# Kernel optimization log

Measured on AMD Instinct MI355X. Metric: run time of the kernel, lower is better.

Reference implementation:

```python
import jax, jax.numpy as jnp
import numpy as np

E = 8        # num_experts
TOPK = 2     # k
D = 1024     # input/output size
H = 4096     # expert hidden size


def setup_inputs() -> dict:
    key = jax.random.key(0)
    ks = jax.random.split(key, 8)
    s = 0.02
    return {
        "hidden_states": jax.random.normal(ks[0], (2, 2048, D), dtype=jnp.float32),
        "Wr": jax.random.normal(ks[1], (D, E), dtype=jnp.float32) * s,
        "br": jnp.zeros((E,), dtype=jnp.float32),
        "gate_bias": jnp.zeros((E,), dtype=jnp.float32),
        "W1": jax.random.normal(ks[2], (E, D, H), dtype=jnp.float32) * s,
        "b1": jnp.zeros((E, H), dtype=jnp.float32),
        "W2": jax.random.normal(ks[3], (E, H, D), dtype=jnp.float32) * s,
        "b2": jnp.zeros((E, D), dtype=jnp.float32),
    }


def reference(hidden_states, Wr, br, gate_bias, W1, b1, W2, b2):
    B, S, Din = hidden_states.shape
    x = hidden_states.reshape(B * S, Din)              # [T, D]
    # Router: logits + gate bias, top-k, softmax over the k selected logits
    logits = x @ Wr + br + gate_bias                   # [T, E]
    top_v, top_i = jax.lax.top_k(logits, TOPK)         # [T, k]
    probs = jax.nn.softmax(top_v, axis=-1)             # [T, k]
    # Scatter top-k probs into dense per-expert gate weights [T, E]
    gate = jnp.einsum("tk,tke->te", probs,
                      jax.nn.one_hot(top_i, E, dtype=probs.dtype))
    # Per-expert MLP (exact gelu, eval mode -> no dropout/noise),
    # weighted-combine; zero gate weight == token not routed to expert.
    out = jnp.zeros((B * S, W2.shape[-1]), dtype=x.dtype)
    for e in range(E):
        h = jax.nn.gelu(x @ W1[e] + b1[e], approximate=False)  # [T, H]
        y = h @ W2[e] + b2[e]                                  # [T, D]
        out = out + gate[:, e:e + 1] * y
    return out.reshape(B, S, -1)
```

## Files before the change

kernel.cpp:

```cpp
#include <hip/hip_runtime.h>
#include <hip/hip_bf16.h>
#include <stdint.h>
#include <stddef.h>


#define T_TOK 4096
#define DIM   1024
#define HID   4096
#define NE    8
#define MT_MAX 40

typedef unsigned short u16;
typedef __bf16 bf16x8 __attribute__((ext_vector_type(8)));
typedef float  f32x4  __attribute__((ext_vector_type(4)));
typedef u16    u16x8  __attribute__((ext_vector_type(8)));

__device__ __forceinline__ u16 f2bf(float f) {
  union { float f; uint32_t u; } v; v.f = f;
  uint32_t u = v.u;
  return (u16)((u + 0x7fffu + ((u >> 16) & 1u)) >> 16);
}

__global__ void router_kernel(const float* __restrict__ x, const float* __restrict__ Wr,
                              const float* __restrict__ br, const float* __restrict__ gb,
                              int* __restrict__ counts, int* __restrict__ lists,
                              float* __restrict__ gate_p) {
  const int t = blockIdx.x * 4 + (threadIdx.x >> 6);
  const int lane = threadIdx.x & 63;
  const float* xr = x + (size_t)t * DIM;
  float acc[NE];
#pragma unroll
  for (int e = 0; e < NE; ++e) acc[e] = 0.f;
#pragma unroll
  for (int i = 0; i < DIM / 64; ++i) {
    const int k = i * 64 + lane;
    const float xv = xr[k];
    const float4 w0 = *reinterpret_cast<const float4*>(Wr + (size_t)k * NE);
    const float4 w1 = *reinterpret_cast<const float4*>(Wr + (size_t)k * NE + 4);
    acc[0] += xv * w0.x; acc[1] += xv * w0.y; acc[2] += xv * w0.z; acc[3] += xv * w0.w;
    acc[4] += xv * w1.x; acc[5] += xv * w1.y; acc[6] += xv * w1.z; acc[7] += xv * w1.w;
  }
#pragma unroll
  for (int off = 32; off >= 1; off >>= 1) {
#pragma unroll
    for (int e = 0; e < NE; ++e) acc[e] += __shfl_xor(acc[e], off);
  }
  if (lane == 0) {
    float lg[NE];
#pragma unroll
    for (int e = 0; e < NE; ++e) lg[e] = acc[e] + br[e] + gb[e];
    int i0 = 0;
#pragma unroll
    for (int e = 1; e < NE; ++e) if (lg[e] > lg[i0]) i0 = e;
    int i1 = (i0 == 0) ? 1 : 0;
#pragma unroll
    for (int e = 0; e < NE; ++e) if (e != i0 && lg[e] > lg[i1]) i1 = e;
    const float ev = expf(lg[i1] - lg[i0]);
    const float p0 = 1.f / (1.f + ev);
    const float p1 = ev / (1.f + ev);
    const int pos0 = atomicAdd(&counts[i0], 1);
    lists[i0 * T_TOK + pos0] = t * 2 + 0;
    const int pos1 = atomicAdd(&counts[i1], 1);
    lists[i1 * T_TOK + pos1] = t * 2 + 1;
    gate_p[t * 2 + 0] = p0;
    gate_p[t * 2 + 1] = p1;
  }
}

__global__ void tile_table_kernel(const int* __restrict__ counts, int* __restrict__ tab) {
  if (threadIdx.x == 0) {
    int tot = 0;
    for (int e = 0; e < NE; ++e) {
      const int c = counts[e];
      const int nt = (c + 255) >> 8;
      for (int i = 0; i < nt && tot < MT_MAX; ++i) {
        tab[tot * 2] = e; tab[tot * 2 + 1] = i * 256; ++tot;
      }
    }
    for (; tot < MT_MAX; ++tot) tab[tot * 2] = -1;
  }
}

__global__ void cvt_x_kernel(const float* __restrict__ in, u16* __restrict__ out, int n8) {
  const int i = blockIdx.x * blockDim.x + threadIdx.x;
  if (i >= n8) return;
  const float4 a = reinterpret_cast<const float4*>(in)[2 * i];
  const float4 b = reinterpret_cast<const float4*>(in)[2 * i + 1];
  u16x8 r;
  r[0] = f2bf(a.x); r[1] = f2bf(a.y); r[2] = f2bf(a.z); r[3] = f2bf(a.w);
  r[4] = f2bf(b.x); r[5] = f2bf(b.y); r[6] = f2bf(b.z); r[7] = f2bf(b.w);
  *reinterpret_cast<u16x8*>(out + (size_t)i * 8) = r;
}

__global__ void cvt_w_kernel(const float* __restrict__ in, u16* __restrict__ out,
                             int K, int N) {
  __shared__ float tile[64][65];
  const int e = blockIdx.z;
  const int n0 = blockIdx.x * 64, k0 = blockIdx.y * 64;
  const int tid = threadIdx.x;
  const float* src = in + (size_t)e * K * N;
#pragma unroll
  for (int r = 0; r < 16; ++r) {
    const int kr = r * 4 + (tid >> 6);
    tile[kr][tid & 63] = src[(size_t)(k0 + kr) * N + n0 + (tid & 63)];
  }
  __syncthreads();
  u16* dst = out + (size_t)e * N * K;
#pragma unroll
  for (int r = 0; r < 8; ++r) {
    const int nr = r * 8 + (tid >> 5);
    const int kc = (tid & 31) * 2;
    ushort2 v;
    v.x = f2bf(tile[kc][nr]);
    v.y = f2bf(tile[kc + 1][nr]);
    *reinterpret_cast<ushort2*>(&dst[(size_t)(n0 + nr) * K + k0 + kc]) = v;
  }
}

__device__ __forceinline__ void ld_afrags(const u16* sm, int cA, int fmh, int wm,
                                          int l15, int swz0, int swz1, bf16x8 af[4][2]) {
#pragma unroll
  for (int f = 0; f < 4; ++f) {
    const int r = fmh * 128 + wm * 64 + f * 16 + l15;
    af[f][0] = *reinterpret_cast<const bf16x8*>(&sm[cA + r * 64 + swz0 * 8]);
    af[f][1] = *reinterpret_cast<const bf16x8*>(&sm[cA + r * 64 + swz1 * 8]);
  }
}
__device__ __forceinline__ void ld_bfrags(const u16* sm, int cA, int nfh, int wn,
                                          int l15, int swz0, int swz1, bf16x8 bfr[2][2]) {
#pragma unroll
  for (int g = 0; g < 2; ++g) {
    const int r = nfh * 128 + wn * 32 + g * 16 + l15;
    bfr[g][0] = *reinterpret_cast<const bf16x8*>(&sm[32768 + cA + r * 64 + swz0 * 8]);
    bfr[g][1] = *reinterpret_cast<const bf16x8*>(&sm[32768 + cA + r * 64 + swz1 * 8]);
  }
}
__device__ __forceinline__ void wr_half(u16* sm, int baseoff, int h, int trow, int wslot,
                                        const bf16x8 v[2]) {
#pragma unroll
  for (int j = 0; j < 2; ++j) {
    const int r = h * 128 + j * 64 + trow;
    *reinterpret_cast<bf16x8*>(&sm[baseoff + r * 64 + wslot * 8]) = v[j];
  }
}

#define PH_SYNC()                                           \
  asm volatile("s_waitcnt lgkmcnt(0)" ::: "memory");        \
  __builtin_amdgcn_s_barrier();                             \
  __builtin_amdgcn_sched_barrier(0);

#define MMQ(FMH, NFH, AF, BF)                                                   \
  __builtin_amdgcn_s_setprio(1);                                                \
  _Pragma("unroll") for (int f_ = 0; f_ < 4; ++f_)                              \
  _Pragma("unroll") for (int g_ = 0; g_ < 2; ++g_)                              \
  _Pragma("unroll") for (int ks_ = 0; ks_ < 2; ++ks_)                           \
    acc[(FMH) * 4 + f_][(NFH) * 2 + g_] =                                       \
        __builtin_amdgcn_mfma_f32_16x16x32_bf16(                                \
            AF[f_][ks_], BF[g_][ks_], acc[(FMH) * 4 + f_][(NFH) * 2 + g_],      \
            0, 0, 0);                                                           \
  __builtin_amdgcn_s_setprio(0);

template <int KT, int NT, int NSPLIT, int PHASE>
__global__ __launch_bounds__(512, 2)
void gemm_kernel(const u16* __restrict__ Abase, const u16* __restrict__ Bt,
                 const float* __restrict__ bias, const int* __restrict__ counts,
                 const int* __restrict__ lists, const float* __restrict__ gate_p,
                 const int* __restrict__ tab,
                 u16* __restrict__ hout, float* __restrict__ yout) {
  const int e = tab[blockIdx.x * 2];
  if (e < 0) return;
  const int m0 = tab[blockIdx.x * 2 + 1];
  const int cnt = counts[e];
  const int n0 = blockIdx.y * 256;
  const int z = blockIdx.z;
  const int kbase = z * (KT / NSPLIT);
  constexpr int nkt = (KT / NSPLIT) / 64;

  const int tid = threadIdx.x;
  const int lane = tid & 63, w = tid >> 6;
  const int wm = w >> 2, wn = w & 3;
  const int l15 = lane & 15, lks = lane >> 4;
  const int rb = l15 & 7;
  const int swz0 = lks ^ rb, swz1 = (4 + lks) ^ rb;

  __shared__ alignas(16) u16 lds[65536];
  __shared__ int rowp[256];

  if (tid < 256) {
    const int idx = m0 + tid;
    rowp[tid] = lists[e * T_TOK + (idx < cnt ? idx : cnt - 1)];
  }
  __syncthreads();

  const int trow = tid >> 3;
  const int tslot = tid & 7;
  const int wslot = tslot ^ (trow & 7);
  const u16* aP[2][2];
  const u16* bP[2][2];
#pragma unroll
  for (int h = 0; h < 2; ++h)
#pragma unroll
    for (int j = 0; j < 2; ++j) {
      const int r = h * 128 + j * 64 + trow;
      const int p = rowp[r];
      const int arow = (PHASE == 1) ? (p >> 1) : p;
      aP[h][j] = Abase + (size_t)arow * KT + kbase + tslot * 8;
      bP[h][j] = Bt + ((size_t)e * NT + n0 + r) * KT + kbase + tslot * 8;
    }

  f32x4 acc[8][4];
#pragma unroll
  for (int a = 0; a < 8; ++a)
#pragma unroll
    for (int b = 0; b < 4; ++b) acc[a][b] = f32x4{0.f, 0.f, 0.f, 0.f};

  bf16x8 aL0[2], aL1[2], bL0[2], bL1[2], af[4][2], bfr[2][2];

  {
    bf16x8 w0[2], w1[2];
#pragma unroll
    for (int j = 0; j < 2; ++j) {
      w0[j]  = *reinterpret_cast<const bf16x8*>(aP[0][j]);
      w1[j]  = *reinterpret_cast<const bf16x8*>(bP[0][j]);
      aL1[j] = *reinterpret_cast<const bf16x8*>(aP[1][j]);
      bL1[j] = *reinterpret_cast<const bf16x8*>(bP[1][j]);
    }
    wr_half(lds, 0, 0, trow, wslot, w0);
    wr_half(lds, 32768, 0, trow, wslot, w1);
  }

#define TILE(C, T)                                                                   \
  {                                                                                  \
    constexpr int cA = (C) * 16384;                                                  \
    constexpr int nA = ((C) ^ 1) * 16384;                                            \
    const int tn = (T) + 1;                                                          \
                                       \
    PH_SYNC();                                                                       \
    ld_afrags(lds, cA, 0, wm, l15, swz0, swz1, af);                                  \
    ld_bfrags(lds, cA, 0, wn, l15, swz0, swz1, bfr);                                 \
    if (tn < nkt) {                                                                  \
      aL0[0] = *reinterpret_cast<const bf16x8*>(aP[0][0] + tn * 64);                 \
      aL0[1] = *reinterpret_cast<const bf16x8*>(aP[0][1] + tn * 64);                 \
    }                                                                                \
    wr_half(lds, 32768 + cA, 1, trow, wslot, bL1);                                   \
    MMQ(0, 0, af, bfr);                                                              \
                                          \
    PH_SYNC();                                                                       \
    ld_bfrags(lds, cA, 1, wn, l15, swz0, swz1, bfr);                                 \
    if (tn < nkt) {                                                                  \
      bL0[0] = *reinterpret_cast<const bf16x8*>(bP[0][0] + tn * 64);                 \
      bL0[1] = *reinterpret_cast<const bf16x8*>(bP[0][1] + tn * 64);                 \
    }                                                                                \
    wr_half(lds, cA, 1, trow, wslot, aL1);                                           \
    MMQ(0, 1, af, bfr);                                                              \
                                      \
    PH_SYNC();                                                                       \
    ld_afrags(lds, cA, 1, wm, l15, swz0, swz1, af);                                  \
    ld_bfrags(lds, cA, 0, wn, l15, swz0, swz1, bfr);                                 \
    if (tn < nkt) {                                                                  \
      bL1[0] = *reinterpret_cast<const bf16x8*>(bP[1][0] + tn * 64);                 \
      bL1[1] = *reinterpret_cast<const bf16x8*>(bP[1][1] + tn * 64);                 \
    }                                                                                \
    wr_half(lds, nA, 0, trow, wslot, aL0);                                           \
    MMQ(1, 0, af, bfr);                                                              \
                            \
    ld_bfrags(lds, cA, 1, wn, l15, swz0, swz1, bfr);                                 \
    if (tn < nkt) {                                                                  \
      aL1[0] = *reinterpret_cast<const bf16x8*>(aP[1][0] + tn * 64);                 \
      aL1[1] = *reinterpret_cast<const bf16x8*>(aP[1][1] + tn * 64);                 \
    }                                                                                \
    wr_half(lds, 32768 + nA, 0, trow, wslot, bL0);                                   \
    MMQ(1, 1, af, bfr);                                                              \
  }

  for (int t = 0; t < nkt; t += 2) {
    TILE(0, t);
    TILE(1, t + 1);
  }
#undef TILE

  const float* bias_e = bias + (size_t)e * NT;
  const float bz = (z == 0) ? 1.f : 0.f;
#pragma unroll
  for (int fm = 0; fm < 8; ++fm) {
    const int rbase = (fm >> 2) * 128 + wm * 64 + (fm & 3) * 16 + (lane >> 4) * 4;
#pragma unroll
    for (int r = 0; r < 4; ++r) {
      const int row = rbase + r;
      if (m0 + row >= cnt) continue;
      const int p = rowp[row];
#pragma unroll
      for (int nf = 0; nf < 4; ++nf) {
        const int n = n0 + (nf >> 1) * 128 + wn * 32 + (nf & 1) * 16 + l15;
        const float v = acc[fm][nf][r];
        if (PHASE == 1) {
          const float vb = v + bias_e[n];
          const float g = 0.5f * vb * (1.0f + erff(vb * 0.70710678118654752f));
          hout[(size_t)p * NT + n] = f2bf(g);
        } else if (PHASE == 2) {
          yout[(size_t)z * T_TOK * 2 * NT + (size_t)p * NT + n] =
              gate_p[p] * (v + bz * bias_e[n]);
        } else {
          atomicAdd(&yout[(size_t)(p >> 1) * NT + n], gate_p[p] * (v + bz * bias_e[n]));
        }
      }
    }
  }
}

__global__ void combine4_kernel(const float* __restrict__ yp, float* __restrict__ out) {
  const int i = blockIdx.x * blockDim.x + threadIdx.x;
  const int t = i >> 8, d4 = i & 255;
  const size_t r0 = (size_t)(2 * t) * 256 + d4;
  const size_t zoff = (size_t)T_TOK * 2 * DIM / 4;
  const float4 a = reinterpret_cast<const float4*>(yp)[r0];
  const float4 b = reinterpret_cast<const float4*>(yp)[r0 + 256];
  const float4 c = reinterpret_cast<const float4*>(yp)[zoff + r0];
  const float4 d = reinterpret_cast<const float4*>(yp)[zoff + r0 + 256];
  float4 o;
  o.x = a.x + b.x + c.x + d.x; o.y = a.y + b.y + c.y + d.y;
  o.z = a.z + b.z + c.z + d.z; o.w = a.w + b.w + c.w + d.w;
  reinterpret_cast<float4*>(out)[i] = o;
}

extern "C" void kernel_launch(void* const* d_in, const int* in_sizes, int n_in,
                              void* d_out, int out_size, void* d_ws, size_t ws_size,
                              hipStream_t stream) {
  const float* x  = (const float*)d_in[0];
  const float* Wr = (const float*)d_in[1];
  const float* br = (const float*)d_in[2];
  const float* gb = (const float*)d_in[3];
  const float* W1 = (const float*)d_in[4];
  const float* b1 = (const float*)d_in[5];
  const float* W2 = (const float*)d_in[6];
  const float* b2 = (const float*)d_in[7];
  float* out = (float*)d_out;

  char* ws = (char*)d_ws;
  size_t off = 0;
  int*   counts = (int*)(ws + off);   off += 256;
  int*   ttab   = (int*)(ws + off);   off += 512;
  int*   lists  = (int*)(ws + off);   off += (size_t)NE * T_TOK * 4;
  float* gate_p = (float*)(ws + off); off += (size_t)T_TOK * 2 * 4;
  u16*   xb     = (u16*)(ws + off);   off += (size_t)T_TOK * DIM * 2;
  u16*   wbuf   = (u16*)(ws + off);   off += (size_t)NE * DIM * HID * 2;
  u16*   hbuf   = (u16*)(ws + off);   off += (size_t)T_TOK * 2 * HID * 2;
  float* ypair  = (float*)(ws + off);
  const size_t need_full = off + (size_t)2 * T_TOK * 2 * DIM * 4;
  const bool use_ypair = (ws_size >= need_full);

  hipMemsetAsync(counts, 0, 32, stream);
  router_kernel<<<T_TOK / 4, 256, 0, stream>>>(x, Wr, br, gb, counts, lists, gate_p);
  tile_table_kernel<<<1, 64, 0, stream>>>(counts, ttab);
  cvt_x_kernel<<<(T_TOK * DIM / 8 + 255) / 256, 256, 0, stream>>>(x, xb, T_TOK * DIM / 8);
  cvt_w_kernel<<<dim3(HID / 64, DIM / 64, NE), 256, 0, stream>>>(W1, wbuf, DIM, HID);
  gemm_kernel<DIM, HID, 1, 1><<<dim3(MT_MAX, HID / 256, 1), 512, 0, stream>>>(
      xb, wbuf, b1, counts, lists, gate_p, ttab, hbuf, nullptr);
  cvt_w_kernel<<<dim3(DIM / 64, HID / 64, NE), 256, 0, stream>>>(W2, wbuf, HID, DIM);
  if (use_ypair) {
    gemm_kernel<HID, DIM, 2, 2><<<dim3(MT_MAX, DIM / 256, 2), 512, 0, stream>>>(
        hbuf, wbuf, b2, counts, lists, gate_p, ttab, nullptr, ypair);
    combine4_kernel<<<T_TOK * DIM / 4 / 256, 256, 0, stream>>>(ypair, out);
  } else {
    hipMemsetAsync(out, 0, (size_t)out_size * 4, stream);
    gemm_kernel<HID, DIM, 2, 3><<<dim3(MT_MAX, DIM / 256, 2), 512, 0, stream>>>(
        hbuf, wbuf, b2, counts, lists, gate_p, ttab, nullptr, out);
  }
}
```

Baseline: 500.2 us.

## Stream GEMM tiles into LDS with direct global_load_lds and restructured warp mapping

Replaces the register-staged global->LDS copy in the expert GEMM main loop with direct global_load_lds async loads, double-buffered across K tiles with vmcnt-based waits and barriers between MFMA quarters. The warp-to-tile mapping also changes: each wave now owns a contiguous 128-row by 64-column block, with the epilogue index math updated to match. The aim is to free VGPRs, drop the LDS write instructions, and overlap memory traffic with MFMA work. The risk is that the hand-tuned vmcnt counts and barrier placement are fragile and could be wrong or stall.

```diff
diff --git a/kernel.cpp b/kernel.cpp
--- a/kernel.cpp
+++ b/kernel.cpp
@@ -19,6 +19,12 @@
   union { float f; uint32_t u; } v; v.f = f;
   uint32_t u = v.u;
   return (u16)((u + 0x7fffu + ((u >> 16) & 1u)) >> 16);
+}
+
+__device__ __forceinline__ void async_load16(const void* g, void* l) {
+  typedef __attribute__((address_space(1))) void GPtr;
+  typedef __attribute__((address_space(3))) void LPtr;
+  __builtin_amdgcn_global_load_lds((GPtr*)g, (LPtr*)l, 16, 0, 0);
 }
 
 __global__ void router_kernel(const float* __restrict__ x, const float* __restrict__ Wr,
@@ -116,49 +122,6 @@
     *reinterpret_cast<ushort2*>(&dst[(size_t)(n0 + nr) * K + k0 + kc]) = v;
   }
 }
-
-__device__ __forceinline__ void ld_afrags(const u16* sm, int cA, int fmh, int wm,
-                                          int l15, int swz0, int swz1, bf16x8 af[4][2]) {
-#pragma unroll
-  for (int f = 0; f < 4; ++f) {
-    const int r = fmh * 128 + wm * 64 + f * 16 + l15;
-    af[f][0] = *reinterpret_cast<const bf16x8*>(&sm[cA + r * 64 + swz0 * 8]);
-    af[f][1] = *reinterpret_cast<const bf16x8*>(&sm[cA + r * 64 + swz1 * 8]);
-  }
-}
-__device__ __forceinline__ void ld_bfrags(const u16* sm, int cA, int nfh, int wn,
-                                          int l15, int swz0, int swz1, bf16x8 bfr[2][2]) {
-#pragma unroll
-  for (int g = 0; g < 2; ++g) {
-    const int r = nfh * 128 + wn * 32 + g * 16 + l15;
-    bfr[g][0] = *reinterpret_cast<const bf16x8*>(&sm[32768 + cA + r * 64 + swz0 * 8]);
-    bfr[g][1] = *reinterpret_cast<const bf16x8*>(&sm[32768 + cA + r * 64 + swz1 * 8]);
-  }
-}
-__device__ __forceinline__ void wr_half(u16* sm, int baseoff, int h, int trow, int wslot,
-                                        const bf16x8 v[2]) {
-#pragma unroll
-  for (int j = 0; j < 2; ++j) {
-    const int r = h * 128 + j * 64 + trow;
-    *reinterpret_cast<bf16x8*>(&sm[baseoff + r * 64 + wslot * 8]) = v[j];
-  }
-}
-
-#define PH_SYNC()                                           \
-  asm volatile("s_waitcnt lgkmcnt(0)" ::: "memory");        \
-  __builtin_amdgcn_s_barrier();                             \
-  __builtin_amdgcn_sched_barrier(0);
-
-#define MMQ(FMH, NFH, AF, BF)                                                   \
-  __builtin_amdgcn_s_setprio(1);                                                \
-  _Pragma("unroll") for (int f_ = 0; f_ < 4; ++f_)                              \
-  _Pragma("unroll") for (int g_ = 0; g_ < 2; ++g_)                              \
-  _Pragma("unroll") for (int ks_ = 0; ks_ < 2; ++ks_)                           \
-    acc[(FMH) * 4 + f_][(NFH) * 2 + g_] =                                       \
-        __builtin_amdgcn_mfma_f32_16x16x32_bf16(                                \
-            AF[f_][ks_], BF[g_][ks_], acc[(FMH) * 4 + f_][(NFH) * 2 + g_],      \
-            0, 0, 0);                                                           \
-  __builtin_amdgcn_s_setprio(0);
 
 template <int KT, int NT, int NSPLIT, int PHASE>
 __global__ __launch_bounds__(512, 2)
@@ -175,13 +138,13 @@
   const int z = blockIdx.z;
   const int kbase = z * (KT / NSPLIT);
   constexpr int nkt = (KT / NSPLIT) / 64;
+  constexpr int niter = nkt / 2;
 
   const int tid = threadIdx.x;
   const int lane = tid & 63, w = tid >> 6;
   const int wm = w >> 2, wn = w & 3;
+  const int bh = wn >> 1, bs = wn & 1;
   const int l15 = lane & 15, lks = lane >> 4;
-  const int rb = l15 & 7;
-  const int swz0 = lks ^ rb, swz1 = (4 + lks) ^ rb;
 
   __shared__ alignas(16) u16 lds[65536];
   __shared__ int rowp[256];
@@ -192,98 +155,134 @@
   }
   __syncthreads();
 
-  const int trow = tid >> 3;
-  const int tslot = tid & 7;
-  const int wslot = tslot ^ (trow & 7);
-  const u16* aP[2][2];
-  const u16* bP[2][2];
+  const int sslot = (tid & 7) ^ ((tid >> 3) & 7);
+  const u16* aPtr[2][2];
+  const u16* bPtr[2][2];
 #pragma unroll
   for (int h = 0; h < 2; ++h)
 #pragma unroll
-    for (int j = 0; j < 2; ++j) {
-      const int r = h * 128 + j * 64 + trow;
+    for (int s = 0; s < 2; ++s) {
+      const int r = h * 128 + s * 64 + (tid >> 3);
       const int p = rowp[r];
       const int arow = (PHASE == 1) ? (p >> 1) : p;
-      aP[h][j] = Abase + (size_t)arow * KT + kbase + tslot * 8;
-      bP[h][j] = Bt + ((size_t)e * NT + n0 + r) * KT + kbase + tslot * 8;
+      aPtr[h][s] = Abase + (size_t)arow * KT + kbase + sslot * 8;
+      bPtr[h][s] = Bt + ((size_t)e * NT + n0 + r) * KT + kbase + sslot * 8;
     }
 
+  int aoff[2];
+#pragma unroll
+  for (int k = 0; k < 2; ++k)
+    aoff[k] = l15 * 64 + (((k * 4 + lks) ^ (l15 & 7)) * 8);
+
   f32x4 acc[8][4];
 #pragma unroll
   for (int a = 0; a < 8; ++a)
 #pragma unroll
     for (int b = 0; b < 4; ++b) acc[a][b] = f32x4{0.f, 0.f, 0.f, 0.f};
 
-  bf16x8 aL0[2], aL1[2], bL0[2], bL1[2], af[4][2], bfr[2][2];
-
-  {
-    bf16x8 w0[2], w1[2];
-#pragma unroll
-    for (int j = 0; j < 2; ++j) {
-      w0[j]  = *reinterpret_cast<const bf16x8*>(aP[0][j]);
-      w1[j]  = *reinterpret_cast<const bf16x8*>(bP[0][j]);
-      aL1[j] = *reinterpret_cast<const bf16x8*>(aP[1][j]);
-      bL1[j] = *reinterpret_cast<const bf16x8*>(bP[1][j]);
-    }
-    wr_half(lds, 0, 0, trow, wslot, w0);
-    wr_half(lds, 32768, 0, trow, wslot, w1);
-  }
-
-#define TILE(C, T)                                                                   \
-  {                                                                                  \
-    constexpr int cA = (C) * 16384;                                                  \
-    constexpr int nA = ((C) ^ 1) * 16384;                                            \
-    const int tn = (T) + 1;                                                          \
-                                       \
-    PH_SYNC();                                                                       \
-    ld_afrags(lds, cA, 0, wm, l15, swz0, swz1, af);                                  \
-    ld_bfrags(lds, cA, 0, wn, l15, swz0, swz1, bfr);                                 \
-    if (tn < nkt) {                                                                  \
-      aL0[0] = *reinterpret_cast<const bf16x8*>(aP[0][0] + tn * 64);                 \
-      aL0[1] = *reinterpret_cast<const bf16x8*>(aP[0][1] + tn * 64);                 \
-    }                                                                                \
-    wr_half(lds, 32768 + cA, 1, trow, wslot, bL1);                                   \
-    MMQ(0, 0, af, bfr);                                                              \
-                                          \
-    PH_SYNC();                                                                       \
-    ld_bfrags(lds, cA, 1, wn, l15, swz0, swz1, bfr);                                 \
-    if (tn < nkt) {                                                                  \
-      bL0[0] = *reinterpret_cast<const bf16x8*>(bP[0][0] + tn * 64);                 \
-      bL0[1] = *reinterpret_cast<const bf16x8*>(bP[0][1] + tn * 64);                 \
-    }                                                                                \
-    wr_half(lds, cA, 1, trow, wslot, aL1);                                           \
-    MMQ(0, 1, af, bfr);                                                              \
-                                      \
-    PH_SYNC();                                                                       \
-    ld_afrags(lds, cA, 1, wm, l15, swz0, swz1, af);                                  \
-    ld_bfrags(lds, cA, 0, wn, l15, swz0, swz1, bfr);                                 \
-    if (tn < nkt) {                                                                  \
-      bL1[0] = *reinterpret_cast<const bf16x8*>(bP[1][0] + tn * 64);                 \
-      bL1[1] = *reinterpret_cast<const bf16x8*>(bP[1][1] + tn * 64);                 \
-    }                                                                                \
-    wr_half(lds, nA, 0, trow, wslot, aL0);                                           \
-    MMQ(1, 0, af, bfr);                                                              \
-                            \
-    ld_bfrags(lds, cA, 1, wn, l15, swz0, swz1, bfr);                                 \
-    if (tn < nkt) {                                                                  \
-      aL1[0] = *reinterpret_cast<const bf16x8*>(aP[1][0] + tn * 64);                 \
-      aL1[1] = *reinterpret_cast<const bf16x8*>(aP[1][1] + tn * 64);                 \
-    }                                                                                \
-    wr_half(lds, 32768 + nA, 0, trow, wslot, bL0);                                   \
-    MMQ(1, 1, af, bfr);                                                              \
-  }
-
-  for (int t = 0; t < nkt; t += 2) {
-    TILE(0, t);
-    TILE(1, t + 1);
-  }
-#undef TILE
+  bf16x8 af[4][2], bfr[4][2];
+
+#define RDA(C, FMH)                                                            \
+  _Pragma("unroll") for (int f_ = 0; f_ < 4; ++f_)                             \
+  _Pragma("unroll") for (int k_ = 0; k_ < 2; ++k_)                             \
+    af[f_][k_] = *reinterpret_cast<const bf16x8*>(                             \
+        &lds[(((C) * 2 + wm) * 2 + (FMH)) * 4096 + f_ * 1024 + aoff[k_]]);
+
+#define RDB(C)                                                                 \
+  _Pragma("unroll") for (int g_ = 0; g_ < 4; ++g_)                             \
+  _Pragma("unroll") for (int k_ = 0; k_ < 2; ++k_)                             \
+    bfr[g_][k_] = *reinterpret_cast<const bf16x8*>(                            \
+        &lds[32768 + (((C) * 2 + bh) * 2 + bs) * 4096 + g_ * 1024 + aoff[k_]]);
+
+#define SGA(C, S, TT)                                                          \
+  _Pragma("unroll") for (int h_ = 0; h_ < 2; ++h_)                             \
+    async_load16(aPtr[h_][S] + (TT) * 64,                                      \
+                 &lds[(((C) * 2 + h_) * 2 + (S)) * 4096 + w * 512]);
+
+#define SGB(C, H, TT)                                                          \
+  _Pragma("unroll") for (int s_ = 0; s_ < 2; ++s_)                             \
+    async_load16(bPtr[H][s_] + (TT) * 64,                                      \
+                 &lds[32768 + (((C) * 2 + (H)) * 2 + s_) * 4096 + w * 512]);
+
+#define MMQ(FMH, FNH)                                                          \
+  _Pragma("unroll") for (int f_ = 0; f_ < 4; ++f_)                             \
+  _Pragma("unroll") for (int g_ = 0; g_ < 2; ++g_)                             \
+  _Pragma("unroll") for (int k_ = 0; k_ < 2; ++k_)                             \
+    acc[(FMH) * 4 + f_][(FNH) * 2 + g_] =                                      \
+        __builtin_amdgcn_mfma_f32_16x16x32_bf16(                               \
+            af[f_][k_], bfr[(FNH) * 2 + g_][k_],                               \
+            acc[(FMH) * 4 + f_][(FNH) * 2 + g_], 0, 0, 0);
+
+#define CORE(FMH, FNH)                                                         \
+  __builtin_amdgcn_s_barrier();                                                \
+  asm volatile("s_waitcnt lgkmcnt(0)" ::: "memory");                           \
+  __builtin_amdgcn_sched_barrier(0);                                           \
+  __builtin_amdgcn_s_setprio(1);                                               \
+  MMQ(FMH, FNH);                                                               \
+  __builtin_amdgcn_s_setprio(0);                                               \
+  __builtin_amdgcn_sched_barrier(0);
+
+#define BAR() __builtin_amdgcn_s_barrier();
+
+#define ITER(T, LAST)                                                          \
+  {                                                                            \
+    RDA(0, 0); RDB(0);                                                         \
+    SGA(1, 1, (T) + 1);                                 \
+    CORE(0, 0) BAR()                                                           \
+    if (!(LAST)) { SGA(0, 0, (T) + 2); }                \
+    CORE(0, 1) BAR()                                                           \
+    RDA(0, 1);                                                                 \
+    if (!(LAST)) { SGB(0, 0, (T) + 2); }                        \
+    CORE(1, 0) BAR()                                                           \
+    if (!(LAST)) { SGB(0, 1, (T) + 2); }                        \
+    CORE(1, 1)                                                                 \
+    if (LAST) { asm volatile("s_waitcnt vmcnt(0)" ::: "memory"); }             \
+    else      { asm volatile("s_waitcnt vmcnt(6)" ::: "memory"); }             \
+    __builtin_amdgcn_sched_barrier(0);                                         \
+    BAR()                                                                      \
+    RDA(1, 0); RDB(1);                                                         \
+    if (!(LAST)) { SGA(0, 1, (T) + 2); }                        \
+    CORE(0, 0) BAR()                                                           \
+    if (!(LAST)) { SGA(1, 0, (T) + 3); }                \
+    CORE(0, 1) BAR()                                                           \
+    RDA(1, 1);                                                                 \
+    if (!(LAST)) { SGB(1, 0, (T) + 3); }                        \
+    CORE(1, 0) BAR()                                                           \
+    if (!(LAST)) { SGB(1, 1, (T) + 3); }                        \
+    CORE(1, 1)                                                                 \
+    if (!(LAST)) {                                                             \
+      asm volatile("s_waitcnt vmcnt(6)" ::: "memory");                         \
+      __builtin_amdgcn_sched_barrier(0);                                       \
+    }                                                                          \
+    BAR()                                                                      \
+  }
+
+  SGA(0, 0, 0); SGB(0, 0, 0); SGB(0, 1, 0); SGA(0, 1, 0);
+  SGA(1, 0, 1); SGB(1, 0, 1); SGB(1, 1, 1);
+  asm volatile("s_waitcnt vmcnt(6)" ::: "memory");
+  __builtin_amdgcn_sched_barrier(0);
+  __builtin_amdgcn_s_barrier();
+
+  for (int it = 0; it < niter - 1; ++it) {
+    const int t = 2 * it;
+    ITER(t, false);
+  }
+  ITER(nkt - 2, true);
+
+#undef ITER
+#undef CORE
+#undef MMQ
+#undef SGB
+#undef SGA
+#undef RDB
+#undef RDA
+#undef BAR
 
   const float* bias_e = bias + (size_t)e * NT;
   const float bz = (z == 0) ? 1.f : 0.f;
 #pragma unroll
   for (int fm = 0; fm < 8; ++fm) {
-    const int rbase = (fm >> 2) * 128 + wm * 64 + (fm & 3) * 16 + (lane >> 4) * 4;
+    const int rbase = wm * 128 + (fm >> 2) * 64 + (fm & 3) * 16 + (lane >> 4) * 4;
 #pragma unroll
     for (int r = 0; r < 4; ++r) {
       const int row = rbase + r;
@@ -291,7 +290,7 @@
       const int p = rowp[row];
 #pragma unroll
       for (int nf = 0; nf < 4; ++nf) {
-        const int n = n0 + (nf >> 1) * 128 + wn * 32 + (nf & 1) * 16 + l15;
+        const int n = n0 + wn * 64 + nf * 16 + l15;
         const float v = acc[fm][nf][r];
         if (PHASE == 1) {
           const float vb = v + bias_e[n];
```

After: 497.9 us. About the same (-0.5%).
